# Performance work log

Hardware: AMD Instinct MI355X
Metric: run time of the kernel (lower is better)

The kernel has to match this reference:

```python
import jax, jax.numpy as jnp
import numpy as np

B, T, D_IN, H, NUM_CLASSES = 1024, 512, 4, 64, 3
G = 4 * H  # gates: i, f, g, o (PyTorch order)


def setup_inputs() -> dict:
    key = jax.random.key(0)
    ks = jax.random.split(key, 32)
    s = 0.1  # small init scale, like PyTorch's 1/sqrt(H) uniform
    inp = {"x": jax.random.normal(ks[0], (B, T, D_IN), jnp.float32)}
    i = 1
    for l in range(4):
        d = D_IN if l == 0 else H
        inp[f"w_ih_{l}"] = s * jax.random.normal(ks[i], (G, d), jnp.float32); i += 1
        inp[f"w_hh_{l}"] = s * jax.random.normal(ks[i], (G, H), jnp.float32); i += 1
        inp[f"b_ih_{l}"] = s * jax.random.normal(ks[i], (G,), jnp.float32); i += 1
        inp[f"b_hh_{l}"] = s * jax.random.normal(ks[i], (G,), jnp.float32); i += 1
    inp["fc1_w"] = s * jax.random.normal(ks[i], (H // 2, H), jnp.float32); i += 1
    inp["fc1_b"] = s * jax.random.normal(ks[i], (H // 2,), jnp.float32); i += 1
    inp["fc2_w"] = s * jax.random.normal(ks[i], (NUM_CLASSES, H // 2), jnp.float32); i += 1
    inp["fc2_b"] = s * jax.random.normal(ks[i], (NUM_CLASSES,), jnp.float32)
    return inp


def _lstm_layer(x, w_ih, w_hh, b_ih, b_hh):
    # x: [B, T, d_in] -> [B, T, H]; PyTorch gate order i, f, g, o.
    b, t, _ = x.shape
    # Precompute input contribution for all timesteps in one GEMM.
    pre = jnp.einsum('btd,gd->tbg', x, w_ih) + (b_ih + b_hh)  # [T, B, 4H]
    h0 = jnp.zeros((b, H), x.dtype)
    c0 = jnp.zeros((b, H), x.dtype)

    def step(carry, p):
        h, c = carry
        gates = p + h @ w_hh.T  # [B, 4H]
        i_g, f_g, g_g, o_g = jnp.split(gates, 4, axis=-1)
        i_g = jax.nn.sigmoid(i_g)
        f_g = jax.nn.sigmoid(f_g)
        g_g = jnp.tanh(g_g)
        o_g = jax.nn.sigmoid(o_g)
        c = f_g * c + i_g * g_g
        h = o_g * jnp.tanh(c)
        return (h, c), h

    _, hs = jax.lax.scan(step, (h0, c0), pre)  # hs: [T, B, H]
    return hs.transpose(1, 0, 2)


def reference(x,
              w_ih_0, w_hh_0, b_ih_0, b_hh_0,
              w_ih_1, w_hh_1, b_ih_1, b_hh_1,
              w_ih_2, w_hh_2, b_ih_2, b_hh_2,
              w_ih_3, w_hh_3, b_ih_3, b_hh_3,
              fc1_w, fc1_b, fc2_w, fc2_b):
    layers = [(w_ih_0, w_hh_0, b_ih_0, b_hh_0),
              (w_ih_1, w_hh_1, b_ih_1, b_hh_1),
              (w_ih_2, w_hh_2, b_ih_2, b_hh_2),
              (w_ih_3, w_hh_3, b_ih_3, b_hh_3)]
    h = x
    for (wi, wh, bi, bh) in layers:
        h = _lstm_layer(h, wi, wh, bi, bh)
    last = h[:, -1, :]                         # [B, H]
    z = jax.nn.relu(last @ fc1_w.T + fc1_b)    # [B, H//2]
    logits = z @ fc2_w.T + fc2_b               # [B, 3]
    return jax.nn.softmax(logits, axis=1)
```

## Files before the change

kernel.cpp:

```cpp
#include <hip/hip_runtime.h>


#define TLEN 512
#define NCH  64
#define AG   __HIP_MEMORY_SCOPE_AGENT
#define SPIN_CAP 2000000
#define LOG2E 1.44269504f
#define TWOLOG2E 2.88539008f

typedef __bf16 bf16x8 __attribute__((ext_vector_type(8)));
typedef float  f32x4  __attribute__((ext_vector_type(4)));

struct Params {
  const float* x;
  const float* wih[4]; const float* whh[4];
  const float* bih[4]; const float* bhh[4];
  const float* fc1w; const float* fc1b;
  const float* fc2w; const float* fc2b;
  float* out; char* ws;
  int CAP; int CM;
};

__device__ __forceinline__ bf16x8 bfzero() {
  union { unsigned long long u[2]; bf16x8 v; } z; z.u[0] = 0ull; z.u[1] = 0ull; return z.v;
}
__device__ __forceinline__ float fast_sigmoid(float x) {
  return __builtin_amdgcn_rcpf(1.f + __expf(-x));
}
__device__ __forceinline__ float fast_tanh(float x) {
  float e = __expf(2.f * x);
  return 1.f - 2.f * __builtin_amdgcn_rcpf(e + 1.f);
}
__device__ __forceinline__ void load_frag_pair(const unsigned short* sb, int l15, int quad,
                                               bf16x8& f0, bf16x8& f1) {
  const unsigned long long* a = (const unsigned long long*)(sb + l15 * 64 + quad * 8);
  const unsigned long long* b = (const unsigned long long*)(sb + l15 * 64 + 32 + quad * 8);
  union { bf16x8 v; unsigned long long u[2]; } c0, c1;
  c0.u[0] = __hip_atomic_load(&a[0], __ATOMIC_RELAXED, AG);
  c0.u[1] = __hip_atomic_load(&a[1], __ATOMIC_RELAXED, AG);
  c1.u[0] = __hip_atomic_load(&b[0], __ATOMIC_RELAXED, AG);
  c1.u[1] = __hip_atomic_load(&b[1], __ATOMIC_RELAXED, AG);
  f0 = c0.v; f1 = c1.v;
}

__global__ __launch_bounds__(512, 2) void lstm_split(Params p)
{
  const int bid   = blockIdx.x;
  const int role  = bid >> 6;
  const int chunk = bid & 63;
  const int b0    = chunk * 16;
  const int tid   = threadIdx.x;
  const int wave  = tid >> 6;
  const int grp   = wave >> 2;
  const int w     = wave & 3;
  const int lane  = tid & 63;
  const int quad  = lane >> 4;
  const int l15   = lane & 15;
  const int L     = role * 2 + grp;

  __shared__ __bf16 tiles[2][2][1024];
  __shared__ float  s_fc1w[2048];
  __shared__ float  s_z[512];
  __shared__ float  s_fc1b[32];
  __shared__ float  s_fc2w[96];
  __shared__ float  s_fc2b[3];
  __shared__ char   anti_pack_pad[64 * 1024];

  if (p.CAP == -12345) anti_pack_pad[tid] = (char)tid;

  int* flagp = (int*)p.ws + chunk * 16;
  int* ackp  = (int*)(p.ws + 16 * 1024) + chunk * 16;
  unsigned short* ringc = (unsigned short*)(p.ws + 32 * 1024) + (size_t)chunk * p.CAP * 1024;
  const int CAP = p.CAP, CM = p.CM;

  bf16x8 wf[4][4];
  float  bias[4];
  {
    const float gsc[4] = { -LOG2E, -LOG2E, TWOLOG2E, -LOG2E };
    const float* wih = p.wih[L];
    const float* whh = p.whh[L];
    const float* bih = p.bih[L];
    const float* bhh = p.bhh[L];
#pragma unroll
    for (int g = 0; g < 4; g++) {
      const float sc = gsc[g];
      int n = g * 64 + w * 16 + l15;
      bias[g] = (bih[n] + bhh[n]) * sc;
      if (L == 0) {
        bf16x8 f = bfzero();
        if (quad == 0) {
#pragma unroll
          for (int j = 0; j < 4; j++) f[j] = (__bf16)(wih[n * 4 + j] * sc);
        }
        wf[g][0] = f; wf[g][1] = bfzero();
      } else {
#pragma unroll
        for (int q = 0; q < 2; q++) {
          const float* s = wih + n * 64 + q * 32 + quad * 8;
          bf16x8 f;
#pragma unroll
          for (int j = 0; j < 8; j++) f[j] = (__bf16)(s[j] * sc);
          wf[g][q] = f;
        }
      }
#pragma unroll
      for (int q = 0; q < 2; q++) {
        const float* s = whh + n * 64 + q * 32 + quad * 8;
        bf16x8 f;
#pragma unroll
        for (int j = 0; j < 8; j++) f[j] = (__bf16)(s[j] * sc);
        wf[g][2 + q] = f;
      }
    }
  }

  { int* ti = (int*)tiles; for (int i = tid; i < 2048; i += 512) ti[i] = 0; }
  float cst[4] = {0.f, 0.f, 0.f, 0.f};

  int W = -1000000000, f_pend = -1000000000;
  int ackW = -1000000000, a_pend = -1000000000;
  bf16x8 xA0 = bfzero(), xA1 = bfzero();
  bf16x8 xB0 = bfzero(), xB1 = bfzero();
  bf16x8 xC0 = bfzero(), xC1 = bfzero();
  float4 xraw = {0.f, 0.f, 0.f, 0.f};

  if (role == 0) {
    if (grp == 0 && quad == 0) {
      const float* xb = p.x + (size_t)(b0 + l15) * TLEN * 4;
      const float4 x0 = *(const float4*)(xb);
      const float4 x1 = *(const float4*)(xb + 4);
      xraw = *(const float4*)(xb + 8);
      bf16x8 f = bfzero();
      f[0] = (__bf16)x0.x; f[1] = (__bf16)x0.y; f[2] = (__bf16)x0.z; f[3] = (__bf16)x0.w;
      xA0 = f;
      bf16x8 g = bfzero();
      g[0] = (__bf16)x1.x; g[1] = (__bf16)x1.y; g[2] = (__bf16)x1.z; g[3] = (__bf16)x1.w;
      xB0 = g;
    }
  } else if (grp == 0) {
    int v = -1000000000, it = 0;
    do {
      if (lane == 0) v = __hip_atomic_load(flagp, __ATOMIC_ACQUIRE, AG);
      v = __shfl(v, 0);
      if (v >= 10) break;
      __builtin_amdgcn_s_sleep(1);
    } while (++it < SPIN_CAP);
    W = v;
    load_frag_pair(ringc,        l15, quad, xA0, xA1);
    load_frag_pair(ringc + 1024, l15, quad, xB0, xB1);
    load_frag_pair(ringc + 2048, l15, quad, xC0, xC1);
  }
  __syncthreads();

  const int SMAX = (role == 0) ? (TLEN + 2) : (TLEN + 1);
  for (int s = 0; s < SMAX; s++) {
    const int t  = s - grp;
    const int pr = s & 1, pw = pr ^ 1;
    unsigned hb[4];

    if ((unsigned)t < (unsigned)TLEN) {
      bf16x8 if0, if1;
      if (grp == 0) { if0 = xA0; if1 = xA1; }
      else {
        const __bf16* src = tiles[pr][0];
        int sg0 = quad ^ (l15 & 7);
        int sg1 = (4 + quad) ^ (l15 & 7);
        if0 = *(const bf16x8*)&src[l15 * 64 + sg0 * 8];
        if1 = *(const bf16x8*)&src[l15 * 64 + sg1 * 8];
      }
      bf16x8 hf0, hf1;
      {
        const __bf16* src = tiles[pr][grp];
        int sg0 = quad ^ (l15 & 7);
        int sg1 = (4 + quad) ^ (l15 & 7);
        hf0 = *(const bf16x8*)&src[l15 * 64 + sg0 * 8];
        hf1 = *(const bf16x8*)&src[l15 * 64 + sg1 * 8];
      }

      f32x4 acc[4];
#pragma unroll
      for (int g = 0; g < 4; g++) { f32x4 a = {bias[g], bias[g], bias[g], bias[g]}; acc[g] = a; }
      if (L == 0) {
#pragma unroll
        for (int g = 0; g < 4; g++)
          acc[g] = __builtin_amdgcn_mfma_f32_16x16x32_bf16(if0, wf[g][0], acc[g], 0, 0, 0);
      } else {
#pragma unroll
        for (int g = 0; g < 4; g++) {
          acc[g] = __builtin_amdgcn_mfma_f32_16x16x32_bf16(if0, wf[g][0], acc[g], 0, 0, 0);
          acc[g] = __builtin_amdgcn_mfma_f32_16x16x32_bf16(if1, wf[g][1], acc[g], 0, 0, 0);
        }
      }
#pragma unroll
      for (int g = 0; g < 4; g++) {
        acc[g] = __builtin_amdgcn_mfma_f32_16x16x32_bf16(hf0, wf[g][2], acc[g], 0, 0, 0);
        acc[g] = __builtin_amdgcn_mfma_f32_16x16x32_bf16(hf1, wf[g][3], acc[g], 0, 0, 0);
      }

      const int col = w * 16 + l15;
      __bf16* dst = tiles[pw][grp];
#pragma unroll
      for (int r = 0; r < 4; r++) {
        float ig = __builtin_amdgcn_rcpf(1.f + __builtin_amdgcn_exp2f(acc[0][r]));
        float fg = __builtin_amdgcn_rcpf(1.f + __builtin_amdgcn_exp2f(acc[1][r]));
        float gg = 1.f - 2.f * __builtin_amdgcn_rcpf(1.f + __builtin_amdgcn_exp2f(acc[2][r]));
        float og = __builtin_amdgcn_rcpf(1.f + __builtin_amdgcn_exp2f(acc[3][r]));
        float c  = fg * cst[r] + ig * gg;
        cst[r] = c;
        float th = 1.f - 2.f * __builtin_amdgcn_rcpf(1.f + __builtin_amdgcn_exp2f(TWOLOG2E * c));
        float h  = og * th;
        __bf16 hbf = (__bf16)h;
        union { __bf16 b; unsigned short s; } cv; cv.b = hbf;
        hb[r] = cv.s;
        int m  = quad * 4 + r;
        int sg = (col >> 3) ^ (m & 7);
        dst[m * 64 + sg * 8 + (col & 7)] = hbf;
      }
    }

    __syncthreads();

    if (role == 0) {
      if (grp == 0) {
        xA0 = xB0;
        if (quad == 0) {
          bf16x8 f = bfzero();
          f[0] = (__bf16)xraw.x; f[1] = (__bf16)xraw.y;
          f[2] = (__bf16)xraw.z; f[3] = (__bf16)xraw.w;
          xB0 = f;
          if (t + 3 < TLEN)
            xraw = *(const float4*)(p.x + ((size_t)(b0 + l15) * TLEN + (t + 3)) * 4);
        }
      }
      if (grp == 1 && (unsigned)t < (unsigned)TLEN) {
        int am = __shfl(a_pend, 0);
        if (am > ackW) ackW = am;
        if (lane == 0) a_pend = __hip_atomic_load(ackp, __ATOMIC_RELAXED, AG);
        if (t >= CAP && ackW < t - CAP + 1) {
          int v = ackW, it = 0;
          do {
            if (lane == 0) v = __hip_atomic_load(ackp, __ATOMIC_ACQUIRE, AG);
            v = __shfl(v, 0);
            if (v >= t - CAP + 1) break;
            __builtin_amdgcn_s_sleep(1);
          } while (++it < SPIN_CAP);
          ackW = v;
        }
        const int col = w * 16 + l15;
        unsigned* rdst = (unsigned*)(ringc + (size_t)(t & CM) * 1024);
#pragma unroll
        for (int r = 0; r < 4; r++) {
          unsigned v = hb[r];
          unsigned o = (unsigned)__shfl_xor((int)v, 1);
          if ((lane & 1) == 0) {
            int m = quad * 4 + r;
            __hip_atomic_store(&rdst[(m * 64 + col) >> 1], v | (o << 16), __ATOMIC_RELAXED, AG);
          }
        }
      }
      if (tid == 0 && s >= 2)
        __hip_atomic_store(flagp, s - 1, __ATOMIC_RELAXED, AG);
    } else {
      if (grp == 0) {
        int fm = __shfl(f_pend, 0);
        if (fm > W) W = fm;
        if (lane == 0) f_pend = __hip_atomic_load(flagp, __ATOMIC_RELAXED, AG);
        xA0 = xB0; xA1 = xB1; xB0 = xC0; xB1 = xC1;
        if (t + 3 < TLEN) {
          if (W < t + 4) {
            int v = W, it = 0;
            do {
              if (lane == 0) v = __hip_atomic_load(flagp, __ATOMIC_ACQUIRE, AG);
              v = __shfl(v, 0);
              if (v >= t + 4) break;
              __builtin_amdgcn_s_sleep(1);
            } while (++it < SPIN_CAP);
            W = v;
          }
          load_frag_pair(ringc + (size_t)((t + 3) & CM) * 1024, l15, quad, xC0, xC1);
        }
      }
      if (tid == 0)
        __hip_atomic_store(ackp, s + 2, __ATOMIC_RELAXED, AG);
    }
  }

  if (role == 1) {
    for (int i = tid; i < 2048; i += 512) s_fc1w[i] = p.fc1w[i];
    if (tid < 32) s_fc1b[tid] = p.fc1b[tid];
    if (tid < 96) s_fc2w[tid] = p.fc2w[tid];
    if (tid < 3)  s_fc2b[tid] = p.fc2b[tid];
    __syncthreads();
    {
      int m = tid >> 5, u = tid & 31;
      float sacc = s_fc1b[u];
      const float* wrow = &s_fc1w[u * 64];
      const __bf16* hfin = tiles[1][1];
#pragma unroll
      for (int k = 0; k < 64; k++) {
        int sg = (k >> 3) ^ (m & 7);
        sacc += (float)hfin[m * 64 + sg * 8 + (k & 7)] * wrow[k];
      }
      s_z[m * 32 + u] = fmaxf(sacc, 0.f);
    }
    __syncthreads();
    if (tid < 16) {
      int m = tid;
      float lg[3];
#pragma unroll
      for (int v = 0; v < 3; v++) {
        float sv = s_fc2b[v];
#pragma unroll
        for (int u = 0; u < 32; u++) sv += s_z[m * 32 + u] * s_fc2w[v * 32 + u];
        lg[v] = sv;
      }
      float mx = fmaxf(lg[0], fmaxf(lg[1], lg[2]));
      float e0 = __expf(lg[0] - mx), e1 = __expf(lg[1] - mx), e2 = __expf(lg[2] - mx);
      float inv = 1.f / (e0 + e1 + e2);
      float* o = p.out + (size_t)(b0 + m) * 3;
      o[0] = e0 * inv; o[1] = e1 * inv; o[2] = e2 * inv;
    }
  }
}

__global__ __launch_bounds__(1024) void lstm_fused(Params p)
{
  const int chunk = blockIdx.x;
  const int b0   = chunk * 16;
  const int tid  = threadIdx.x;
  const int wave = tid >> 6;
  const int L    = wave >> 2;
  const int w    = wave & 3;
  const int lane = tid & 63;
  const int quad = lane >> 4;
  const int l15  = lane & 15;

  __shared__ __bf16 tiles[2][5][16 * 64];
  __shared__ float  s_fc1w[2048];
  __shared__ float  s_z[512];
  __shared__ float  s_fc1b[32];
  __shared__ float  s_fc2w[96];
  __shared__ float  s_fc2b[3];

  bf16x8 wf[4][4];
  float  bias[4];
  {
    const float* wih = p.wih[L];
    const float* whh = p.whh[L];
    const float* bih = p.bih[L];
    const float* bhh = p.bhh[L];
#pragma unroll
    for (int g = 0; g < 4; g++) {
      int n = g * 64 + w * 16 + l15;
      bias[g] = bih[n] + bhh[n];
      if (L == 0) {
        bf16x8 f = bfzero();
        if (quad == 0) {
#pragma unroll
          for (int j = 0; j < 4; j++) f[j] = (__bf16)wih[n * 4 + j];
        }
        wf[g][0] = f; wf[g][1] = bfzero();
      } else {
#pragma unroll
        for (int q = 0; q < 2; q++) {
          const float* s = wih + n * 64 + q * 32 + quad * 8;
          bf16x8 f;
#pragma unroll
          for (int j = 0; j < 8; j++) f[j] = (__bf16)s[j];
          wf[g][q] = f;
        }
      }
#pragma unroll
      for (int q = 0; q < 2; q++) {
        const float* s = whh + n * 64 + q * 32 + quad * 8;
        bf16x8 f;
#pragma unroll
        for (int j = 0; j < 8; j++) f[j] = (__bf16)s[j];
        wf[g][2 + q] = f;
      }
    }
  }

  { int* ti = (int*)tiles; for (int i = tid; i < 5120; i += 1024) ti[i] = 0; }
  float cst[4] = {0.f, 0.f, 0.f, 0.f};

  if (wave == 0 && quad == 0) {
    const float4 xv = *(const float4*)(p.x + ((size_t)(b0 + l15) * TLEN) * 4);
    __bf16 v[4] = {(__bf16)xv.x, (__bf16)xv.y, (__bf16)xv.z, (__bf16)xv.w};
    *(float2*)&tiles[0][0][l15 * 64 + (l15 & 7) * 8] = *(float2*)v;
  }
  __syncthreads();

  for (int s = 0; s < TLEN + 3; s++) {
    const int t  = s - L;
    const int pr = s & 1;
    const int pw = pr ^ 1;

    if ((unsigned)t < (unsigned)TLEN) {
      const __bf16* in  = tiles[pr][L];
      const __bf16* own = tiles[pr][L + 1];
      const int sg0 = quad ^ (l15 & 7);
      const int sg1 = (4 + quad) ^ (l15 & 7);
      bf16x8 xf0 = *(const bf16x8*)&in [l15 * 64 + sg0 * 8];
      bf16x8 xf1 = *(const bf16x8*)&in [l15 * 64 + sg1 * 8];
      bf16x8 hf0 = *(const bf16x8*)&own[l15 * 64 + sg0 * 8];
      bf16x8 hf1 = *(const bf16x8*)&own[l15 * 64 + sg1 * 8];

      f32x4 acc[4];
#pragma unroll
      for (int g = 0; g < 4; g++) { f32x4 a = {bias[g], bias[g], bias[g], bias[g]}; acc[g] = a; }
#pragma unroll
      for (int g = 0; g < 4; g++) {
        acc[g] = __builtin_amdgcn_mfma_f32_16x16x32_bf16(xf0, wf[g][0], acc[g], 0, 0, 0);
        acc[g] = __builtin_amdgcn_mfma_f32_16x16x32_bf16(xf1, wf[g][1], acc[g], 0, 0, 0);
        acc[g] = __builtin_amdgcn_mfma_f32_16x16x32_bf16(hf0, wf[g][2], acc[g], 0, 0, 0);
        acc[g] = __builtin_amdgcn_mfma_f32_16x16x32_bf16(hf1, wf[g][3], acc[g], 0, 0, 0);
      }

      if (wave == 0 && quad == 0 && t + 1 < TLEN) {
        const float4 xv = *(const float4*)(p.x + ((size_t)(b0 + l15) * TLEN + (t + 1)) * 4);
        __bf16 v[4] = {(__bf16)xv.x, (__bf16)xv.y, (__bf16)xv.z, (__bf16)xv.w};
        *(float2*)&tiles[pw][0][l15 * 64 + (l15 & 7) * 8] = *(float2*)v;
      }

      const int col = w * 16 + l15;
      __bf16* dst = tiles[pw][L + 1];
#pragma unroll
      for (int r = 0; r < 4; r++) {
        float ig = fast_sigmoid(acc[0][r]);
        float fg = fast_sigmoid(acc[1][r]);
        float gg = fast_tanh(acc[2][r]);
        float og = fast_sigmoid(acc[3][r]);
        float c = fg * cst[r] + ig * gg;
        cst[r] = c;
        float h = og * fast_tanh(c);
        int m  = quad * 4 + r;
        int sg = (col >> 3) ^ (m & 7);
        dst[m * 64 + sg * 8 + (col & 7)] = (__bf16)h;
      }
    }
    __syncthreads();
  }

  for (int i = tid; i < 2048; i += 1024) s_fc1w[i] = p.fc1w[i];
  if (tid < 32) s_fc1b[tid] = p.fc1b[tid];
  if (tid < 96) s_fc2w[tid] = p.fc2w[tid];
  if (tid < 3)  s_fc2b[tid] = p.fc2b[tid];
  __syncthreads();
  if (tid < 512) {
    int m = tid >> 5, u = tid & 31;
    float sacc = s_fc1b[u];
    const float* wrow = &s_fc1w[u * 64];
    const __bf16* hfin = tiles[1][4];
#pragma unroll
    for (int k = 0; k < 64; k++) {
      int sg = (k >> 3) ^ (m & 7);
      sacc += (float)hfin[m * 64 + sg * 8 + (k & 7)] * wrow[k];
    }
    s_z[m * 32 + u] = fmaxf(sacc, 0.f);
  }
  __syncthreads();
  if (tid < 16) {
    int m = tid;
    float lg[3];
#pragma unroll
    for (int v = 0; v < 3; v++) {
      float sv = s_fc2b[v];
#pragma unroll
      for (int u = 0; u < 32; u++) sv += s_z[m * 32 + u] * s_fc2w[v * 32 + u];
      lg[v] = sv;
    }
    float mx = fmaxf(lg[0], fmaxf(lg[1], lg[2]));
    float e0 = __expf(lg[0] - mx), e1 = __expf(lg[1] - mx), e2 = __expf(lg[2] - mx);
    float inv = 1.f / (e0 + e1 + e2);
    float* o = p.out + (size_t)(b0 + m) * 3;
    o[0] = e0 * inv; o[1] = e1 * inv; o[2] = e2 * inv;
  }
}

extern "C" void kernel_launch(void* const* d_in, const int* in_sizes, int n_in,
                              void* d_out, int out_size, void* d_ws, size_t ws_size,
                              hipStream_t stream)
{
  (void)in_sizes; (void)n_in; (void)out_size;
  Params p;
  p.x = (const float*)d_in[0];
  for (int l = 0; l < 4; l++) {
    p.wih[l] = (const float*)d_in[1 + 4 * l];
    p.whh[l] = (const float*)d_in[2 + 4 * l];
    p.bih[l] = (const float*)d_in[3 + 4 * l];
    p.bhh[l] = (const float*)d_in[4 + 4 * l];
  }
  p.fc1w = (const float*)d_in[17];
  p.fc1b = (const float*)d_in[18];
  p.fc2w = (const float*)d_in[19];
  p.fc2b = (const float*)d_in[20];
  p.out = (float*)d_out;
  p.ws  = (char*)d_ws;

  const size_t avail = (ws_size > 32768) ? (ws_size - 32768) : 0;
  int CAP = 1;
  while (CAP < 64 && (size_t)(CAP * 2) * (NCH * 2048ull) <= avail) CAP <<= 1;

  if (CAP >= 16) {
    p.CAP = CAP; p.CM = CAP - 1;
    hipLaunchKernelGGL(lstm_split, dim3(128), dim3(512), 0, stream, p);
  } else {
    p.CAP = 0; p.CM = 0;
    hipLaunchKernelGGL(lstm_fused, dim3(NCH), dim3(1024), 0, stream, p);
  }
}
```

Baseline: 882.0 us.

## Add four-stage layer pipeline kernel with one block per layer-chunk

Adds lstm_pipe4, which launches 256 blocks of 256 threads, one block per (layer, batch chunk). Each layer streams its bf16 hidden states to the next layer through per-chunk ring buffers in workspace, coordinated by flag and ack counters. This replaces the two-block split that put two layers in each block, so all four layers run as a wavefront pipeline across more CUs. It also removes the LDS padding from lstm_split and lowers the spin cap. In exchange it uses more cross-block synchronisation and a larger workspace, and it depends on all 256 blocks being co-resident.

```diff
diff --git a/kernel.cpp b/kernel.cpp
--- a/kernel.cpp
+++ b/kernel.cpp
@@ -4,7 +4,7 @@
 #define TLEN 512
 #define NCH  64
 #define AG   __HIP_MEMORY_SCOPE_AGENT
-#define SPIN_CAP 2000000
+#define SPIN_CAP 150000
 #define LOG2E 1.44269504f
 #define TWOLOG2E 2.88539008f
 
@@ -18,7 +18,7 @@
   const float* fc1w; const float* fc1b;
   const float* fc2w; const float* fc2b;
   float* out; char* ws;
-  int CAP; int CM;
+  int CAP; int CM; int GATE;
 };
 
 __device__ __forceinline__ bf16x8 bfzero() {
@@ -43,6 +43,274 @@
   f0 = c0.v; f1 = c1.v;
 }
 
+__global__ __launch_bounds__(256, 1) void lstm_pipe4(Params p)
+{
+  const int bid   = blockIdx.x;
+  const int L     = bid >> 6;
+  const int chunk = bid & 63;
+  const int b0    = chunk * 16;
+  const int tid   = threadIdx.x;
+  const int w     = tid >> 6;
+  const int lane  = tid & 63;
+  const int quad  = lane >> 4;
+  const int l15   = lane & 15;
+
+  __shared__ __bf16 tiles[2][1024];
+  __shared__ float  s_fc1w[2048];
+  __shared__ float  s_z[512];
+  __shared__ float  s_fc1b[32];
+  __shared__ float  s_fc2w[96];
+  __shared__ float  s_fc2b[3];
+
+  const int CAP = p.CAP, CM = p.CM, GATE = p.GATE;
+  const int iidx = (L > 0) ? ((L - 1) * 64 + chunk) : 0;
+  const int oidx = (L < 3) ? (L * 64 + chunk) : 0;
+  int* iflag = (int*)p.ws + iidx * 16;
+  int* oflag = (int*)p.ws + oidx * 16;
+  int* iack  = (int*)(p.ws + 16 * 1024) + iidx * 16;
+  int* oack  = (int*)(p.ws + 16 * 1024) + oidx * 16;
+  unsigned short* inring  = (unsigned short*)(p.ws + 32 * 1024) + (size_t)iidx * CAP * 1024;
+  unsigned short* outring = (unsigned short*)(p.ws + 32 * 1024) + (size_t)oidx * CAP * 1024;
+
+  bf16x8 wf[4][4];
+  float  bias[4];
+  {
+    const float gsc[4] = { -LOG2E, -LOG2E, TWOLOG2E, -LOG2E };
+    const float* wih = p.wih[L];
+    const float* whh = p.whh[L];
+    const float* bih = p.bih[L];
+    const float* bhh = p.bhh[L];
+#pragma unroll
+    for (int g = 0; g < 4; g++) {
+      const float sc = gsc[g];
+      int n = g * 64 + w * 16 + l15;
+      bias[g] = (bih[n] + bhh[n]) * sc;
+      if (L == 0) {
+        bf16x8 f = bfzero();
+        if (quad == 0) {
+#pragma unroll
+          for (int j = 0; j < 4; j++) f[j] = (__bf16)(wih[n * 4 + j] * sc);
+        }
+        wf[g][0] = f; wf[g][1] = bfzero();
+      } else {
+#pragma unroll
+        for (int q = 0; q < 2; q++) {
+          const float* s = wih + n * 64 + q * 32 + quad * 8;
+          bf16x8 f;
+#pragma unroll
+          for (int j = 0; j < 8; j++) f[j] = (__bf16)(s[j] * sc);
+          wf[g][q] = f;
+        }
+      }
+#pragma unroll
+      for (int q = 0; q < 2; q++) {
+        const float* s = whh + n * 64 + q * 32 + quad * 8;
+        bf16x8 f;
+#pragma unroll
+        for (int j = 0; j < 8; j++) f[j] = (__bf16)(s[j] * sc);
+        wf[g][2 + q] = f;
+      }
+    }
+  }
+
+  { int* ti = (int*)tiles; for (int i = tid; i < 1024; i += 256) ti[i] = 0; }
+  float cst[4] = {0.f, 0.f, 0.f, 0.f};
+
+  int W = -1000000000, f_pend = -1000000000;
+  int ackW = -1000000000, a_pend = -1000000000;
+  bf16x8 xA0 = bfzero(), xA1 = bfzero();
+  bf16x8 xB0 = bfzero(), xB1 = bfzero();
+  bf16x8 xC0 = bfzero(), xC1 = bfzero();
+  float4 xraw = {0.f, 0.f, 0.f, 0.f};
+
+  if (L == 0) {
+    if (quad == 0) {
+      const float* xb = p.x + (size_t)(b0 + l15) * TLEN * 4;
+      const float4 x0 = *(const float4*)(xb);
+      const float4 x1 = *(const float4*)(xb + 4);
+      xraw = *(const float4*)(xb + 8);
+      bf16x8 f = bfzero();
+      f[0] = (__bf16)x0.x; f[1] = (__bf16)x0.y; f[2] = (__bf16)x0.z; f[3] = (__bf16)x0.w;
+      xA0 = f;
+      bf16x8 g = bfzero();
+      g[0] = (__bf16)x1.x; g[1] = (__bf16)x1.y; g[2] = (__bf16)x1.z; g[3] = (__bf16)x1.w;
+      xB0 = g;
+    }
+  } else {
+    int v = -1000000000, it = 0;
+    do {
+      if (lane == 0) v = __hip_atomic_load(iflag, __ATOMIC_ACQUIRE, AG);
+      v = __shfl(v, 0);
+      if (v >= GATE) break;
+      __builtin_amdgcn_s_sleep(1);
+    } while (++it < SPIN_CAP);
+    W = v;
+    load_frag_pair(inring,        l15, quad, xA0, xA1);
+    load_frag_pair(inring + 1024, l15, quad, xB0, xB1);
+    load_frag_pair(inring + 2048, l15, quad, xC0, xC1);
+  }
+  __syncthreads();
+
+  for (int s = 0; s < TLEN + 2; s++) {
+    const int t  = s;
+    const int pr = s & 1, pw = pr ^ 1;
+    unsigned hb[4];
+
+    if (t < TLEN) {
+      bf16x8 hf0, hf1;
+      {
+        const __bf16* src = tiles[pr];
+        int sg0 = quad ^ (l15 & 7);
+        int sg1 = (4 + quad) ^ (l15 & 7);
+        hf0 = *(const bf16x8*)&src[l15 * 64 + sg0 * 8];
+        hf1 = *(const bf16x8*)&src[l15 * 64 + sg1 * 8];
+      }
+
+      f32x4 acc[4];
+#pragma unroll
+      for (int g = 0; g < 4; g++) { f32x4 a = {bias[g], bias[g], bias[g], bias[g]}; acc[g] = a; }
+      if (L == 0) {
+#pragma unroll
+        for (int g = 0; g < 4; g++)
+          acc[g] = __builtin_amdgcn_mfma_f32_16x16x32_bf16(xA0, wf[g][0], acc[g], 0, 0, 0);
+      } else {
+#pragma unroll
+        for (int g = 0; g < 4; g++) {
+          acc[g] = __builtin_amdgcn_mfma_f32_16x16x32_bf16(xA0, wf[g][0], acc[g], 0, 0, 0);
+          acc[g] = __builtin_amdgcn_mfma_f32_16x16x32_bf16(xA1, wf[g][1], acc[g], 0, 0, 0);
+        }
+      }
+#pragma unroll
+      for (int g = 0; g < 4; g++) {
+        acc[g] = __builtin_amdgcn_mfma_f32_16x16x32_bf16(hf0, wf[g][2], acc[g], 0, 0, 0);
+        acc[g] = __builtin_amdgcn_mfma_f32_16x16x32_bf16(hf1, wf[g][3], acc[g], 0, 0, 0);
+      }
+
+      const int col = w * 16 + l15;
+      __bf16* dst = tiles[pw];
+#pragma unroll
+      for (int r = 0; r < 4; r++) {
+        float ig = __builtin_amdgcn_rcpf(1.f + __builtin_amdgcn_exp2f(acc[0][r]));
+        float fg = __builtin_amdgcn_rcpf(1.f + __builtin_amdgcn_exp2f(acc[1][r]));
+        float gg = 1.f - 2.f * __builtin_amdgcn_rcpf(1.f + __builtin_amdgcn_exp2f(acc[2][r]));
+        float og = __builtin_amdgcn_rcpf(1.f + __builtin_amdgcn_exp2f(acc[3][r]));
+        float c  = fg * cst[r] + ig * gg;
+        cst[r] = c;
+        float th = 1.f - 2.f * __builtin_amdgcn_rcpf(1.f + __builtin_amdgcn_exp2f(TWOLOG2E * c));
+        float h  = og * th;
+        __bf16 hbf = (__bf16)h;
+        union { __bf16 b; unsigned short s; } cv; cv.b = hbf;
+        hb[r] = cv.s;
+        int m  = quad * 4 + r;
+        int sg = (col >> 3) ^ (m & 7);
+        dst[m * 64 + sg * 8 + (col & 7)] = hbf;
+      }
+    }
+
+    __syncthreads();
+
+    if (L == 0) {
+      xA0 = xB0;
+      if (quad == 0) {
+        bf16x8 f = bfzero();
+        f[0] = (__bf16)xraw.x; f[1] = (__bf16)xraw.y;
+        f[2] = (__bf16)xraw.z; f[3] = (__bf16)xraw.w;
+        xB0 = f;
+        if (t + 3 < TLEN)
+          xraw = *(const float4*)(p.x + ((size_t)(b0 + l15) * TLEN + (t + 3)) * 4);
+      }
+    } else {
+      int fm = __shfl(f_pend, 0);
+      if (fm > W) W = fm;
+      if (lane == 0) f_pend = __hip_atomic_load(iflag, __ATOMIC_RELAXED, AG);
+      xA0 = xB0; xA1 = xB1; xB0 = xC0; xB1 = xC1;
+      if (t + 3 < TLEN) {
+        if (W < t + 4) {
+          int v = W, it = 0;
+          do {
+            if (lane == 0) v = __hip_atomic_load(iflag, __ATOMIC_ACQUIRE, AG);
+            v = __shfl(v, 0);
+            if (v >= t + 4) break;
+            __builtin_amdgcn_s_sleep(1);
+          } while (++it < SPIN_CAP);
+          W = v;
+        }
+        load_frag_pair(inring + (size_t)((t + 3) & CM) * 1024, l15, quad, xC0, xC1);
+      }
+      if (tid == 0)
+        __hip_atomic_store(iack, s + 2, __ATOMIC_RELAXED, AG);
+    }
+
+    if (L < 3) {
+      if (t < TLEN) {
+        int am = __shfl(a_pend, 0);
+        if (am > ackW) ackW = am;
+        if (lane == 0) a_pend = __hip_atomic_load(oack, __ATOMIC_RELAXED, AG);
+        if (t >= CAP && ackW < t - CAP + 1) {
+          int v = ackW, it = 0;
+          do {
+            if (lane == 0) v = __hip_atomic_load(oack, __ATOMIC_ACQUIRE, AG);
+            v = __shfl(v, 0);
+            if (v >= t - CAP + 1) break;
+            __builtin_amdgcn_s_sleep(1);
+          } while (++it < SPIN_CAP);
+          ackW = v;
+        }
+        const int col = w * 16 + l15;
+        unsigned* rdst = (unsigned*)(outring + (size_t)(t & CM) * 1024);
+#pragma unroll
+        for (int r = 0; r < 4; r++) {
+          unsigned v = hb[r];
+          unsigned o = (unsigned)__shfl_xor((int)v, 1);
+          if ((lane & 1) == 0) {
+            int m = quad * 4 + r;
+            __hip_atomic_store(&rdst[(m * 64 + col) >> 1], v | (o << 16), __ATOMIC_RELAXED, AG);
+          }
+        }
+      }
+      if (tid == 0 && s >= 2)
+        __hip_atomic_store(oflag, s - 1, __ATOMIC_RELAXED, AG);
+    }
+  }
+
+  if (L == 3) {
+    for (int i = tid; i < 2048; i += 256) s_fc1w[i] = p.fc1w[i];
+    if (tid < 32) s_fc1b[tid] = p.fc1b[tid];
+    if (tid < 96) s_fc2w[tid] = p.fc2w[tid];
+    if (tid < 3)  s_fc2b[tid] = p.fc2b[tid];
+    __syncthreads();
+    for (int i = tid; i < 512; i += 256) {
+      int m = i >> 5, u = i & 31;
+      float sacc = s_fc1b[u];
+      const float* wrow = &s_fc1w[u * 64];
+      const __bf16* hfin = tiles[0];
+#pragma unroll
+      for (int k = 0; k < 64; k++) {
+        int sg = (k >> 3) ^ (m & 7);
+        sacc += (float)hfin[m * 64 + sg * 8 + (k & 7)] * wrow[k];
+      }
+      s_z[m * 32 + u] = fmaxf(sacc, 0.f);
+    }
+    __syncthreads();
+    if (tid < 16) {
+      int m = tid;
+      float lg[3];
+#pragma unroll
+      for (int v = 0; v < 3; v++) {
+        float sv = s_fc2b[v];
+#pragma unroll
+        for (int u = 0; u < 32; u++) sv += s_z[m * 32 + u] * s_fc2w[v * 32 + u];
+        lg[v] = sv;
+      }
+      float mx = fmaxf(lg[0], fmaxf(lg[1], lg[2]));
+      float e0 = __expf(lg[0] - mx), e1 = __expf(lg[1] - mx), e2 = __expf(lg[2] - mx);
+      float inv = 1.f / (e0 + e1 + e2);
+      float* o = p.out + (size_t)(b0 + m) * 3;
+      o[0] = e0 * inv; o[1] = e1 * inv; o[2] = e2 * inv;
+    }
+  }
+}
+
 __global__ __launch_bounds__(512, 2) void lstm_split(Params p)
 {
   const int bid   = blockIdx.x;
@@ -64,9 +332,6 @@
   __shared__ float  s_fc1b[32];
   __shared__ float  s_fc2w[96];
   __shared__ float  s_fc2b[3];
-  __shared__ char   anti_pack_pad[64 * 1024];
-
-  if (p.CAP == -12345) anti_pack_pad[tid] = (char)tid;
 
   int* flagp = (int*)p.ws + chunk * 16;
   int* ackp  = (int*)(p.ws + 16 * 1024) + chunk * 16;
@@ -499,14 +764,22 @@
   p.ws  = (char*)d_ws;
 
   const size_t avail = (ws_size > 32768) ? (ws_size - 32768) : 0;
-  int CAP = 1;
-  while (CAP < 64 && (size_t)(CAP * 2) * (NCH * 2048ull) <= avail) CAP <<= 1;
-
-  if (CAP >= 16) {
-    p.CAP = CAP; p.CM = CAP - 1;
+
+  int CAP3 = 1;
+  while (CAP3 < 64 && (size_t)(CAP3 * 2) * (192ull * 2048ull) <= avail) CAP3 <<= 1;
+  int CAP1 = 1;
+  while (CAP1 < 64 && (size_t)(CAP1 * 2) * (64ull * 2048ull) <= avail) CAP1 <<= 1;
+
+  if (CAP3 >= 8) {
+    p.CAP = CAP3; p.CM = CAP3 - 1;
+    int g = CAP3 - 3; if (g > 10) g = 10;
+    p.GATE = g;
+    hipLaunchKernelGGL(lstm_pipe4, dim3(256), dim3(256), 0, stream, p);
+  } else if (CAP1 >= 16) {
+    p.CAP = CAP1; p.CM = CAP1 - 1; p.GATE = 10;
     hipLaunchKernelGGL(lstm_split, dim3(128), dim3(512), 0, stream, p);
   } else {
-    p.CAP = 0; p.CM = 0;
+    p.CAP = 0; p.CM = 0; p.GATE = 0;
     hipLaunchKernelGGL(lstm_fused, dim3(NCH), dim3(1024), 0, stream, p);
   }
 }
```

After: 1.250 ms. 41.7% more time.
